# Kernel tuning notes

Measured on AMD Instinct MI355X. Metric: run time of the kernel, lower is better.

The kernel has to match this reference:

```python
import jax, jax.numpy as jnp
from jax import lax
import numpy as np

P = 2          # cost exponent: C(x,y) = |x-y|^p / p
BLUR = 0.05    # final epsilon = BLUR**P
SCALING = 0.5  # geomloss epsilon-scaling factor


def _cost(x, y):
    # squared Euclidean distance / 2  (geomloss p=2 cost), shape [N, M]
    sq = jnp.sum(x * x, axis=1)[:, None] + jnp.sum(y * y, axis=1)[None, :] - 2.0 * (x @ y.T)
    return jnp.maximum(sq, 0.0) * 0.5


def _softmin(eps, C, h):
    # h: log-weights (+ potential/eps) over columns of C; returns [rows]
    return -eps * jax.nn.logsumexp(h[None, :] - C / eps, axis=1)


def setup_inputs() -> dict:
    key = jax.random.key(0)
    k1, k2 = jax.random.split(key)
    N, M, D = 8192, 8192, 64
    g = jax.random.normal(k1, (N, D), jnp.float32)
    Y = jax.random.normal(k2, (M, D), jnp.float32) + 1.0  # shifted target measure
    # geomloss epsilon_schedule: diameter**p annealed by SCALING**p down to BLUR**p
    xy = np.concatenate([np.asarray(g), np.asarray(Y)], axis=0)
    diameter = float(np.linalg.norm(xy.max(0) - xy.min(0)))
    eps_list = ([diameter ** P]
                + [float(np.exp(e)) for e in np.arange(P * np.log(diameter), P * np.log(BLUR), P * np.log(SCALING))]
                + [BLUR ** P])
    return {"g": g, "Y": Y, "eps_list": jnp.asarray(eps_list, jnp.float32)}


def reference(g, Y, eps_list):
    x, y = g, Y
    N, M = x.shape[0], y.shape[0]
    a_log = jnp.full((N,), -jnp.log(jnp.float32(N)), x.dtype)  # uniform log-weights
    b_log = jnp.full((M,), -jnp.log(jnp.float32(M)), y.dtype)

    C_xy, C_yx = _cost(x, y), _cost(y, x)
    C_xx, C_yy = _cost(x, x), _cost(y, y)
    # Sinkhorn loop runs on detached costs (geomloss runs it under no_grad)
    sg = lax.stop_gradient
    Cxy_s, Cyx_s, Cxx_s, Cyy_s = sg(C_xy), sg(C_yx), sg(C_xx), sg(C_yy)

    eps0 = eps_list[0]
    f_aa = _softmin(eps0, Cxx_s, a_log)
    g_bb = _softmin(eps0, Cyy_s, b_log)
    g_ab = _softmin(eps0, Cyx_s, a_log)
    f_ba = _softmin(eps0, Cxy_s, b_log)

    def step(carry, eps):
        f_aa, g_bb, g_ab, f_ba = carry
        ft = _softmin(eps, Cxy_s, b_log + g_ab / eps)
        gt = _softmin(eps, Cyx_s, a_log + f_ba / eps)
        ftaa = _softmin(eps, Cxx_s, a_log + f_aa / eps)
        gtbb = _softmin(eps, Cyy_s, b_log + g_bb / eps)
        # symmetrized (averaged) dual updates, as in geomloss
        return (0.5 * (f_aa + ftaa), 0.5 * (g_bb + gtbb),
                0.5 * (g_ab + gt), 0.5 * (f_ba + ft)), None

    (f_aa, g_bb, g_ab, f_ba), _ = lax.scan(step, (f_aa, g_bb, g_ab, f_ba), eps_list)

    # last extrapolation at eps = blur**p: differentiable costs, detached potentials
    eps = eps_list[-1]
    f_ba_f = _softmin(eps, C_xy, sg(b_log + g_ab / eps))
    g_ab_f = _softmin(eps, C_yx, sg(a_log + f_ba / eps))
    f_aa_f = _softmin(eps, C_xx, sg(a_log + f_aa / eps))
    g_bb_f = _softmin(eps, C_yy, sg(b_log + g_bb / eps))

    # S_eps(alpha, beta) = <alpha, f_ba - f_aa> + <beta, g_ab - g_bb> (uniform weights)
    return jnp.mean(f_ba_f - f_aa_f) + jnp.mean(g_ab_f - g_bb_f)
```

## Files before the change

### kernel.cpp

```cpp
#include <hip/hip_runtime.h>
#include <math.h>

#define D 64
#define BR 128
#define NCHUNK 16
#define YLD 72
#define LOG2E 1.4426950408889634f
#define LN2   0.6931471805599453f

typedef __attribute__((ext_vector_type(8))) __bf16 bf16x8;
typedef __attribute__((ext_vector_type(4))) float  floatx4;
typedef __attribute__((ext_vector_type(2))) float  floatx2;

static __device__ __forceinline__ float exp2fast(float x) {
#if __has_builtin(__builtin_amdgcn_exp2f)
    return __builtin_amdgcn_exp2f(x);
#else
    return exp2f(x);
#endif
}
static __device__ __forceinline__ float log2fast(float x) {
#if __has_builtin(__builtin_amdgcn_logf)
    return __builtin_amdgcn_logf(x);
#else
    return log2f(x);
#endif
}
static __device__ __forceinline__ float max3f(float a, float b, float c) {
    return fmaxf(fmaxf(a, b), c);
}

static __device__ __forceinline__ unsigned short f2bf_rne(float f) {
    unsigned u = __float_as_uint(f);
    return (unsigned short)((u + 0x7fffu + ((u >> 16) & 1u)) >> 16);
}

struct OpDesc {
    const unsigned short* xh;
    const unsigned short* yh;
    const float* cc;
    const float* sqn_col;
    float* pm; float* ps;
    int n_rows, n_cols, symmetric, pad;
};
struct P4 { OpDesc op[4]; };

struct MDesc {
    const float* pm; const float* ps;
    const float* sqn_row;
    const float* oldpot;
    float* newpot;
    float* ccout;
    float wlog_c;
    int n_rows, mix, pad;
};
struct M4 { MDesc op[4]; };

__global__ void cvt_kernel(const float* __restrict__ x,
                           unsigned short* __restrict__ xh, int n_elem8)
{
    int i = blockIdx.x * blockDim.x + threadIdx.x;
    if (i >= n_elem8) return;
    const float4* xp = (const float4*)x;
    float4 v0 = xp[i * 2], v1 = xp[i * 2 + 1];
    float v[8] = {v0.x, v0.y, v0.z, v0.w, v1.x, v1.y, v1.z, v1.w};
    unsigned h[8];
#pragma unroll
    for (int k = 0; k < 8; ++k) h[k] = f2bf_rne(v[k]);
    uint4 ph;
    ph.x = h[0] | (h[1] << 16); ph.y = h[2] | (h[3] << 16);
    ph.z = h[4] | (h[5] << 16); ph.w = h[6] | (h[7] << 16);
    ((uint4*)xh)[i] = ph;
}

__global__ void sqnorm_kernel(const float* __restrict__ x, float* __restrict__ sqn, int n)
{
    int i = blockIdx.x * blockDim.x + threadIdx.x;
    if (i >= n) return;
    const float4* xp = (const float4*)(x + (size_t)i * D);
    float sum = 0.0f;
#pragma unroll
    for (int k = 0; k < D / 4; ++k) {
        float4 v = xp[k];
        sum += v.x * v.x + v.y * v.y + v.z * v.z + v.w * v.w;
    }
    sqn[i] = 0.5f * sum;
}

__global__ void init_cc_kernel(const float* __restrict__ sqn_x, const float* __restrict__ sqn_y,
                               float* cc0, float* cc1, float* cc2, float* cc3,
                               const float* __restrict__ eps_list,
                               float a_log, float b_log, int N, int M)
{
    int i = blockIdx.x * blockDim.x + threadIdx.x;
    float inv_e0 = 1.0f / eps_list[0];
    if (i < M) { float v = (b_log - sqn_y[i] * inv_e0) * LOG2E; cc0[i] = v; cc3[i] = v; }
    if (i < N) { float v = (a_log - sqn_x[i] * inv_e0) * LOG2E; cc1[i] = v; cc2[i] = v; }
}

__global__ __launch_bounds__(256)
void softmin_mfma4(P4 p4, const float* __restrict__ eps_list, int eps_idx)
{
    __shared__ __bf16 yth[128 * YLD];

    const OpDesc o = p4.op[blockIdx.z];
    const int t    = threadIdx.x;
    const int lane = t & 63;
    const int w    = t >> 6;
    const int lx   = lane & 15;
    const int q    = lane >> 4;
    const int row0 = blockIdx.x * BR;
    const int chunk = blockIdx.y;
    const int cols_per_chunk = o.n_cols / NCHUNK;
    const int nsub = cols_per_chunk / 128;

    const float eps     = eps_list[eps_idx];
    const float inv_eps = 1.0f / eps;
    const float scale2  = inv_eps * LOG2E;
    const floatx2 s2v   = (floatx2){scale2, scale2};
    const floatx4 Z4    = (floatx4){0.f, 0.f, 0.f, 0.f};

    bf16x8 ah[2][2];
    {
        const int r0 = row0 + w * 32;
#pragma unroll
        for (int rt = 0; rt < 2; ++rt)
#pragma unroll
            for (int ks = 0; ks < 2; ++ks)
                ah[rt][ks] = *(const bf16x8*)(o.xh + (size_t)(r0 + rt * 16 + lx) * D + ks * 32 + q * 8);
    }

    const int diag_blk = o.symmetric && ((row0 / cols_per_chunk) == chunk);
    float sqr[8];
    if (diag_blk) {
#pragma unroll
        for (int idx = 0; idx < 8; ++idx) {
            int row = row0 + w * 32 + (idx >> 2) * 16 + q * 4 + (idx & 3);
            sqr[idx] = o.sqn_col[row];
        }
    }

    float m[8], s[8];
#pragma unroll
    for (int i = 0; i < 8; ++i) { m[i] = -__builtin_inff(); s[i] = 0.0f; }

    for (int sub = 0; sub < nsub; ++sub) {
        const int col0 = chunk * cols_per_chunk + sub * 128;

        __syncthreads();
        {
            const uint4* gh = (const uint4*)(o.yh + (size_t)col0 * D);
#pragma unroll
            for (int i = 0; i < 4; ++i) {
                int c = t + i * 256;
                int row = c >> 3, part = c & 7;
                uint4 vh = gh[c];
                *(uint4*)(&yth[row * YLD + part * 8]) = vh;
            }
        }
        __syncthreads();

        float cc[8];
#pragma unroll
        for (int ct = 0; ct < 8; ++ct) cc[ct] = o.cc[col0 + ct * 16 + lx];

        floatx4 acc[8][2];
#pragma unroll
        for (int ct = 0; ct < 8; ++ct) {
            const int cl = ct * 16 + lx;
            bf16x8 bh0 = *(const bf16x8*)&yth[cl * YLD + q * 8];
            bf16x8 bh1 = *(const bf16x8*)&yth[cl * YLD + 32 + q * 8];
#pragma unroll
            for (int rt = 0; rt < 2; ++rt) {
                floatx4 a = __builtin_amdgcn_mfma_f32_16x16x32_bf16(ah[rt][0], bh0, Z4, 0, 0, 0);
                acc[ct][rt] = __builtin_amdgcn_mfma_f32_16x16x32_bf16(ah[rt][1], bh1, a, 0, 0, 0);
            }
        }

        if (diag_blk && col0 == row0) {
#pragma unroll
            for (int rt = 0; rt < 2; ++rt)
#pragma unroll
                for (int r = 0; r < 4; ++r) {
                    if (lx == q * 4 + r) {
                        const float v = 2.0f * sqr[rt * 4 + r];
#pragma unroll
                        for (int ct = 0; ct < 8; ++ct)
                            if (ct == w * 2 + rt) acc[ct][rt][r] = v;
                    }
                }
        }

        floatx2 ccv[4];
#pragma unroll
        for (int cp = 0; cp < 4; ++cp)
            ccv[cp] = (floatx2){cc[cp * 2], cc[cp * 2 + 1]};

#pragma unroll
        for (int rt = 0; rt < 2; ++rt)
#pragma unroll
            for (int r = 0; r < 4; ++r) {
                const int idx = rt * 4 + r;
                floatx2 zv[4];
#pragma unroll
                for (int cp = 0; cp < 4; ++cp) {
                    floatx2 av = (floatx2){acc[cp * 2][rt][r], acc[cp * 2 + 1][rt][r]};
                    zv[cp] = __builtin_elementwise_fma(av, s2v, ccv[cp]);
                }
                float M = max3f(zv[0].x, zv[0].y, zv[1].x);
                M = max3f(M, zv[1].y, zv[2].x);
                M = max3f(M, zv[2].y, zv[3].x);
                M = max3f(M, zv[3].y, m[idx]);
                const floatx2 Mv = (floatx2){M, M};
                floatx2 sv = (floatx2){0.f, 0.f};
#pragma unroll
                for (int cp = 0; cp < 4; ++cp) {
                    floatx2 d = zv[cp] - Mv;
                    sv += (floatx2){exp2fast(d.x), exp2fast(d.y)};
                }
                s[idx] = fmaf(s[idx], exp2fast(m[idx] - M), sv.x + sv.y);
                m[idx] = M;
            }
    }

#pragma unroll
    for (int idx = 0; idx < 8; ++idx) {
        float mm = m[idx], ss = s[idx];
#pragma unroll
        for (int d = 1; d < 16; d <<= 1) {
            float mo = __shfl_xor(mm, d, 64);
            float so = __shfl_xor(ss, d, 64);
            float M = fmaxf(mm, mo);
            ss = ss * exp2fast(mm - M) + so * exp2fast(mo - M);
            mm = M;
        }
        m[idx] = mm; s[idx] = ss;
    }
    if (lx == 0) {
#pragma unroll
        for (int idx = 0; idx < 8; ++idx) {
            const int rt = idx >> 2, r = idx & 3;
            const int row = row0 + w * 32 + rt * 16 + q * 4 + r;
            o.pm[chunk * o.n_rows + row] = m[idx];
            o.ps[chunk * o.n_rows + row] = s[idx];
        }
    }
}

__global__ void softmin_merge4(M4 m4, const float* __restrict__ eps_list,
                               int eps_idx, int eps_idx_next)
{
    const MDesc o = m4.op[blockIdx.y];
    int i = blockIdx.x * blockDim.x + threadIdx.x;
    if (i >= o.n_rows) return;
    const float eps = eps_list[eps_idx];
    float M = -__builtin_inff();
    for (int c = 0; c < NCHUNK; ++c) M = fmaxf(M, o.pm[c * o.n_rows + i]);
    float S = 0.0f;
    for (int c = 0; c < NCHUNK; ++c) S += o.ps[c * o.n_rows + i] * exp2fast(o.pm[c * o.n_rows + i] - M);
    const float sq = o.sqn_row[i];
    float val = sq - eps * LN2 * (M + log2fast(S));
    float nv = o.mix ? 0.5f * (o.oldpot[i] + val) : val;
    o.newpot[i] = nv;
    if (o.ccout) {
        float inv_en = 1.0f / eps_list[eps_idx_next];
        o.ccout[i] = (o.wlog_c + (nv - sq) * inv_en) * LOG2E;
    }
}

__global__ void final_reduce(const float* __restrict__ f_ba_f, const float* __restrict__ f_aa_f,
                             const float* __restrict__ g_ab_f, const float* __restrict__ g_bb_f,
                             int n, int mcount, float* __restrict__ out)
{
    __shared__ float red[256];
    float s1 = 0.0f, s2 = 0.0f;
    for (int i = threadIdx.x; i < n; i += 256)      s1 += (f_ba_f[i] - f_aa_f[i]);
    for (int i = threadIdx.x; i < mcount; i += 256) s2 += (g_ab_f[i] - g_bb_f[i]);
    red[threadIdx.x] = s1 / (float)n + s2 / (float)mcount;
    __syncthreads();
    for (int off = 128; off > 0; off >>= 1) {
        if (threadIdx.x < off) red[threadIdx.x] += red[threadIdx.x + off];
        __syncthreads();
    }
    if (threadIdx.x == 0) out[0] = red[0];
}

extern "C" void kernel_launch(void* const* d_in, const int* in_sizes, int n_in,
                              void* d_out, int out_size, void* d_ws, size_t ws_size,
                              hipStream_t stream)
{
    const float* g        = (const float*)d_in[0];
    const float* Y        = (const float*)d_in[1];
    const float* eps_list = (const float*)d_in[2];
    const int N = in_sizes[0] / D;
    const int M = in_sizes[1] / D;
    const int L = in_sizes[2];
    const float a_log = -logf((float)N);
    const float b_log = -logf((float)M);
    const int NM = (N > M) ? N : M;
    const size_t PMS = (size_t)NCHUNK * NM;

    unsigned short* us = (unsigned short*)d_ws;
    unsigned short* gxh = us; us += (size_t)N * D;
    unsigned short* gyh = us; us += (size_t)M * D;

    float* ws = (float*)us;
    float* sqn_x = ws; ws += N;
    float* sqn_y = ws; ws += M;
    float* fba[2]; fba[0] = ws; ws += N; fba[1] = ws; ws += N;
    float* gab[2]; gab[0] = ws; ws += M; gab[1] = ws; ws += M;
    float* fa[2];  fa[0]  = ws; ws += N; fa[1]  = ws; ws += N;
    float* gb[2];  gb[0]  = ws; ws += M; gb[1]  = ws; ws += M;
    float* f_ba_f = ws; ws += N;
    float* g_ab_f = ws; ws += M;
    float* f_aa_f = ws; ws += N;
    float* g_bb_f = ws; ws += M;
    float* cc[2][4];
    for (int pbuf = 0; pbuf < 2; ++pbuf)
        for (int i = 0; i < 4; ++i) { cc[pbuf][i] = ws; ws += NM; }
    float* pm = ws; ws += 4 * PMS;
    float* psb = ws; ws += 4 * PMS;

    sqnorm_kernel<<<(N + 255) / 256, 256, 0, stream>>>(g, sqn_x, N);
    sqnorm_kernel<<<(M + 255) / 256, 256, 0, stream>>>(Y, sqn_y, M);
    cvt_kernel<<<(N * D / 8 + 255) / 256, 256, 0, stream>>>(g, gxh, N * D / 8);
    cvt_kernel<<<(M * D / 8 + 255) / 256, 256, 0, stream>>>(Y, gyh, M * D / 8);
    init_cc_kernel<<<(NM + 255) / 256, 256, 0, stream>>>(sqn_x, sqn_y,
        cc[0][0], cc[0][1], cc[0][2], cc[0][3], eps_list, a_log, b_log, N, M);

    auto phase = [&](int eidx, int eidx_next, int mix, int cur, int ccp, int writecc,
                     float* out0, float* out1, float* out2, float* out3) {
        P4 p;
        p.op[0] = { gxh, gyh, cc[ccp][0], sqn_y, pm + 0 * PMS, psb + 0 * PMS, N, M, 0, 0 };
        p.op[1] = { gyh, gxh, cc[ccp][1], sqn_x, pm + 1 * PMS, psb + 1 * PMS, M, N, 0, 0 };
        p.op[2] = { gxh, gxh, cc[ccp][2], sqn_x, pm + 2 * PMS, psb + 2 * PMS, N, N, 1, 0 };
        p.op[3] = { gyh, gyh, cc[ccp][3], sqn_y, pm + 3 * PMS, psb + 3 * PMS, M, M, 1, 0 };
        softmin_mfma4<<<dim3(NM / BR, NCHUNK, 4), 256, 0, stream>>>(p, eps_list, eidx);

        M4 mm;
        mm.op[0] = { pm + 0 * PMS, psb + 0 * PMS, sqn_x, fba[cur], out0,
                     writecc ? cc[ccp ^ 1][1] : nullptr, a_log, N, mix, 0 };
        mm.op[1] = { pm + 1 * PMS, psb + 1 * PMS, sqn_y, gab[cur], out1,
                     writecc ? cc[ccp ^ 1][0] : nullptr, b_log, M, mix, 0 };
        mm.op[2] = { pm + 2 * PMS, psb + 2 * PMS, sqn_x, fa[cur], out2,
                     writecc ? cc[ccp ^ 1][2] : nullptr, a_log, N, mix, 0 };
        mm.op[3] = { pm + 3 * PMS, psb + 3 * PMS, sqn_y, gb[cur], out3,
                     writecc ? cc[ccp ^ 1][3] : nullptr, b_log, M, mix, 0 };
        softmin_merge4<<<dim3((NM + 255) / 256, 4), 256, 0, stream>>>(mm, eps_list, eidx, eidx_next);
    };

    phase(0, 0, 0, 0, 0, 1, fba[0], gab[0], fa[0], gb[0]);
    int cur = 0, ccp = 1;

    for (int k = 0; k < L; ++k) {
        int en = (k + 1 < L) ? (k + 1) : (L - 1);
        phase(k, en, 1, cur, ccp, 1, fba[cur ^ 1], gab[cur ^ 1], fa[cur ^ 1], gb[cur ^ 1]);
        cur ^= 1; ccp ^= 1;
    }

    phase(L - 1, L - 1, 0, cur, ccp, 0, f_ba_f, g_ab_f, f_aa_f, g_bb_f);

    final_reduce<<<1, 256, 0, stream>>>(f_ba_f, f_aa_f, g_ab_f, g_bb_f, N, M, (float*)d_out);
}
```

Before: 1.290 ms.

## Skip negligible softmin chunks using bounds from previous iteration's potentials

```diff
diff --git a/kernel.cpp b/kernel.cpp
--- a/kernel.cpp
+++ b/kernel.cpp
@@ -7,6 +7,7 @@
 #define YLD 72
 #define LOG2E 1.4426950408889634f
 #define LN2   0.6931471805599453f
+#define SAFE_MARGIN 200.0f
 
 typedef __attribute__((ext_vector_type(8))) __bf16 bf16x8;
 typedef __attribute__((ext_vector_type(4))) float  floatx4;
@@ -41,6 +42,8 @@
     const float* cc;
     const float* sqn_col;
     float* pm; float* ps;
+    const int* keep;
+    float wlog_col;
     int n_rows, n_cols, symmetric, pad;
 };
 struct P4 { OpDesc op[4]; };
@@ -51,6 +54,7 @@
     const float* oldpot;
     float* newpot;
     float* ccout;
+    float* dpout;
     float wlog_c;
     int n_rows, mix, pad;
 };
@@ -98,19 +102,86 @@
     if (i < N) { float v = (a_log - sqn_x[i] * inv_e0) * LOG2E; cc1[i] = v; cc2[i] = v; }
 }
 
+__global__ void plan_chunk(const float* __restrict__ dp0, const float* __restrict__ dp1,
+                           const float* __restrict__ dp2, const float* __restrict__ dp3,
+                           float* __restrict__ dmax, float* __restrict__ dmin,
+                           int c0, int c1, int c2, int c3)
+{
+    __shared__ float smx[256], smn[256];
+    const int op = blockIdx.y, c = blockIdx.x, t = threadIdx.x;
+    const float* dp = (op == 0) ? dp0 : (op == 1) ? dp1 : (op == 2) ? dp2 : dp3;
+    const int nc = (op == 0) ? c0 : (op == 1) ? c1 : (op == 2) ? c2 : c3;
+    const int cpc = nc / NCHUNK;
+    float mx = -__builtin_inff(), mn = __builtin_inff();
+    for (int i = t; i < cpc; i += 256) {
+        float v = dp[c * cpc + i];
+        mx = fmaxf(mx, v); mn = fminf(mn, v);
+    }
+    smx[t] = mx; smn[t] = mn;
+    __syncthreads();
+    for (int off = 128; off > 0; off >>= 1) {
+        if (t < off) { smx[t] = fmaxf(smx[t], smx[t + off]); smn[t] = fminf(smn[t], smn[t + off]); }
+        __syncthreads();
+    }
+    if (t == 0) { dmax[op * NCHUNK + c] = smx[0]; dmin[op * NCHUNK + c] = smn[0]; }
+}
+
+__global__ void plan_keep(P4 p4, const float* __restrict__ eps_list, int eps_prev, int eps_cur,
+                          const float* __restrict__ dmax, const float* __restrict__ dmin,
+                          int* __restrict__ keepbuf, int rbmax, int trust_all)
+{
+    __shared__ int flags[NCHUNK];
+    const int op = blockIdx.y, rb = blockIdx.x, t = threadIdx.x;
+    const OpDesc o = p4.op[op];
+    if (rb >= o.n_rows / BR) return;
+    const int row = rb * BR + t;
+    int* kb = keepbuf + ((size_t)op * rbmax + rb) * NCHUNK;
+
+    const float ep = eps_list[eps_prev], ec = eps_list[eps_cur];
+    const float r = ep / ec;
+    const float base = LOG2E * (1.0f - r) * o.wlog_col;
+    const float sc = LOG2E / ec;
+
+    float up[NCHUNK];
+    float glb = -__builtin_inff();
+#pragma unroll
+    for (int c = 0; c < NCHUNK; ++c) {
+        const int oldk = trust_all ? 1 : kb[c];
+        const float pmv = o.pm[c * o.n_rows + row];
+        up[c] = r * pmv + base + dmax[op * NCHUNK + c] * sc;
+        if (oldk) {
+            float lo = r * pmv + base + dmin[op * NCHUNK + c] * sc;
+            glb = fmaxf(glb, lo);
+        }
+    }
+    if (t < NCHUNK) flags[t] = 0;
+    __syncthreads();
+    const float thr = glb - SAFE_MARGIN;
+#pragma unroll
+    for (int c = 0; c < NCHUNK; ++c)
+        if (up[c] >= thr) flags[c] = 1;
+    __syncthreads();
+#pragma unroll
+    for (int c = 0; c < NCHUNK; ++c)
+        if (!flags[c]) { o.pm[c * o.n_rows + row] = up[c]; o.ps[c * o.n_rows + row] = 0.0f; }
+    if (t < NCHUNK) kb[t] = flags[t];
+}
+
 __global__ __launch_bounds__(256)
 void softmin_mfma4(P4 p4, const float* __restrict__ eps_list, int eps_idx)
 {
     __shared__ __bf16 yth[128 * YLD];
 
     const OpDesc o = p4.op[blockIdx.z];
+    const int chunk = blockIdx.y;
+    if (o.keep && o.keep[blockIdx.x * NCHUNK + chunk] == 0) return;
+
     const int t    = threadIdx.x;
     const int lane = t & 63;
     const int w    = t >> 6;
     const int lx   = lane & 15;
     const int q    = lane >> 4;
     const int row0 = blockIdx.x * BR;
-    const int chunk = blockIdx.y;
     const int cols_per_chunk = o.n_cols / NCHUNK;
     const int nsub = cols_per_chunk / 128;
 
@@ -215,8 +286,8 @@
                 floatx2 sv = (floatx2){0.f, 0.f};
 #pragma unroll
                 for (int cp = 0; cp < 4; ++cp) {
-                    floatx2 d = zv[cp] - Mv;
-                    sv += (floatx2){exp2fast(d.x), exp2fast(d.y)};
+                    floatx2 dd = zv[cp] - Mv;
+                    sv += (floatx2){exp2fast(dd.x), exp2fast(dd.y)};
                 }
                 s[idx] = fmaf(s[idx], exp2fast(m[idx] - M), sv.x + sv.y);
                 m[idx] = M;
@@ -234,15 +305,11 @@
             ss = ss * exp2fast(mm - M) + so * exp2fast(mo - M);
             mm = M;
         }
-        m[idx] = mm; s[idx] = ss;
-    }
-    if (lx == 0) {
-#pragma unroll
-        for (int idx = 0; idx < 8; ++idx) {
+        if (lx == 0) {
             const int rt = idx >> 2, r = idx & 3;
             const int row = row0 + w * 32 + rt * 16 + q * 4 + r;
-            o.pm[chunk * o.n_rows + row] = m[idx];
-            o.ps[chunk * o.n_rows + row] = s[idx];
+            o.pm[chunk * o.n_rows + row] = mm;
+            o.ps[chunk * o.n_rows + row] = ss;
         }
     }
 }
@@ -260,12 +327,14 @@
     for (int c = 0; c < NCHUNK; ++c) S += o.ps[c * o.n_rows + i] * exp2fast(o.pm[c * o.n_rows + i] - M);
     const float sq = o.sqn_row[i];
     float val = sq - eps * LN2 * (M + log2fast(S));
-    float nv = o.mix ? 0.5f * (o.oldpot[i] + val) : val;
+    float pold = o.mix ? o.oldpot[i] : 0.0f;
+    float nv = o.mix ? 0.5f * (pold + val) : val;
     o.newpot[i] = nv;
     if (o.ccout) {
         float inv_en = 1.0f / eps_list[eps_idx_next];
         o.ccout[i] = (o.wlog_c + (nv - sq) * inv_en) * LOG2E;
     }
+    if (o.dpout) o.dpout[i] = nv - pold;
 }
 
 __global__ void final_reduce(const float* __restrict__ f_ba_f, const float* __restrict__ f_aa_f,
@@ -298,6 +367,7 @@
     const float a_log = -logf((float)N);
     const float b_log = -logf((float)M);
     const int NM = (N > M) ? N : M;
+    const int rbmax = NM / BR;
     const size_t PMS = (size_t)NCHUNK * NM;
 
     unsigned short* us = (unsigned short*)d_ws;
@@ -318,8 +388,13 @@
     float* cc[2][4];
     for (int pbuf = 0; pbuf < 2; ++pbuf)
         for (int i = 0; i < 4; ++i) { cc[pbuf][i] = ws; ws += NM; }
+    float* dpc[4];
+    for (int i = 0; i < 4; ++i) { dpc[i] = ws; ws += NM; }
+    float* dmax = ws; ws += 4 * NCHUNK;
+    float* dmin = ws; ws += 4 * NCHUNK;
     float* pm = ws; ws += 4 * PMS;
     float* psb = ws; ws += 4 * PMS;
+    int* keepbuf = (int*)ws;
 
     sqnorm_kernel<<<(N + 255) / 256, 256, 0, stream>>>(g, sqn_x, N);
     sqnorm_kernel<<<(M + 255) / 256, 256, 0, stream>>>(Y, sqn_y, M);
@@ -329,36 +404,50 @@
         cc[0][0], cc[0][1], cc[0][2], cc[0][3], eps_list, a_log, b_log, N, M);
 
     auto phase = [&](int eidx, int eidx_next, int mix, int cur, int ccp, int writecc,
-                     float* out0, float* out1, float* out2, float* out3) {
+                     float* out0, float* out1, float* out2, float* out3,
+                     int use_plan, int eps_prev, int trust_all) {
         P4 p;
-        p.op[0] = { gxh, gyh, cc[ccp][0], sqn_y, pm + 0 * PMS, psb + 0 * PMS, N, M, 0, 0 };
-        p.op[1] = { gyh, gxh, cc[ccp][1], sqn_x, pm + 1 * PMS, psb + 1 * PMS, M, N, 0, 0 };
-        p.op[2] = { gxh, gxh, cc[ccp][2], sqn_x, pm + 2 * PMS, psb + 2 * PMS, N, N, 1, 0 };
-        p.op[3] = { gyh, gyh, cc[ccp][3], sqn_y, pm + 3 * PMS, psb + 3 * PMS, M, M, 1, 0 };
+        const int* k0 = use_plan ? keepbuf + 0 * (size_t)rbmax * NCHUNK : nullptr;
+        const int* k1 = use_plan ? keepbuf + 1 * (size_t)rbmax * NCHUNK : nullptr;
+        const int* k2 = use_plan ? keepbuf + 2 * (size_t)rbmax * NCHUNK : nullptr;
+        const int* k3 = use_plan ? keepbuf + 3 * (size_t)rbmax * NCHUNK : nullptr;
+        p.op[0] = { gxh, gyh, cc[ccp][0], sqn_y, pm + 0 * PMS, psb + 0 * PMS, k0, b_log, N, M, 0, 0 };
+        p.op[1] = { gyh, gxh, cc[ccp][1], sqn_x, pm + 1 * PMS, psb + 1 * PMS, k1, a_log, M, N, 0, 0 };
+        p.op[2] = { gxh, gxh, cc[ccp][2], sqn_x, pm + 2 * PMS, psb + 2 * PMS, k2, a_log, N, N, 1, 0 };
+        p.op[3] = { gyh, gyh, cc[ccp][3], sqn_y, pm + 3 * PMS, psb + 3 * PMS, k3, b_log, M, M, 1, 0 };
+
+        if (use_plan) {
+            plan_chunk<<<dim3(NCHUNK, 4), 256, 0, stream>>>(dpc[0], dpc[1], dpc[2], dpc[3],
+                                                            dmax, dmin, M, N, N, M);
+            plan_keep<<<dim3(rbmax, 4), 128, 0, stream>>>(p, eps_list, eps_prev, eidx,
+                                                          dmax, dmin, keepbuf, rbmax, trust_all);
+        }
         softmin_mfma4<<<dim3(NM / BR, NCHUNK, 4), 256, 0, stream>>>(p, eps_list, eidx);
 
         M4 mm;
         mm.op[0] = { pm + 0 * PMS, psb + 0 * PMS, sqn_x, fba[cur], out0,
-                     writecc ? cc[ccp ^ 1][1] : nullptr, a_log, N, mix, 0 };
+                     writecc ? cc[ccp ^ 1][1] : nullptr, writecc ? dpc[1] : nullptr, a_log, N, mix, 0 };
         mm.op[1] = { pm + 1 * PMS, psb + 1 * PMS, sqn_y, gab[cur], out1,
-                     writecc ? cc[ccp ^ 1][0] : nullptr, b_log, M, mix, 0 };
+                     writecc ? cc[ccp ^ 1][0] : nullptr, writecc ? dpc[0] : nullptr, b_log, M, mix, 0 };
         mm.op[2] = { pm + 2 * PMS, psb + 2 * PMS, sqn_x, fa[cur], out2,
-                     writecc ? cc[ccp ^ 1][2] : nullptr, a_log, N, mix, 0 };
+                     writecc ? cc[ccp ^ 1][2] : nullptr, writecc ? dpc[2] : nullptr, a_log, N, mix, 0 };
         mm.op[3] = { pm + 3 * PMS, psb + 3 * PMS, sqn_y, gb[cur], out3,
-                     writecc ? cc[ccp ^ 1][3] : nullptr, b_log, M, mix, 0 };
+                     writecc ? cc[ccp ^ 1][3] : nullptr, writecc ? dpc[3] : nullptr, b_log, M, mix, 0 };
         softmin_merge4<<<dim3((NM + 255) / 256, 4), 256, 0, stream>>>(mm, eps_list, eidx, eidx_next);
     };
 
-    phase(0, 0, 0, 0, 0, 1, fba[0], gab[0], fa[0], gb[0]);
+    phase(0, 0, 0, 0, 0, 1, fba[0], gab[0], fa[0], gb[0], 0, 0, 0);
     int cur = 0, ccp = 1;
 
     for (int k = 0; k < L; ++k) {
         int en = (k + 1 < L) ? (k + 1) : (L - 1);
-        phase(k, en, 1, cur, ccp, 1, fba[cur ^ 1], gab[cur ^ 1], fa[cur ^ 1], gb[cur ^ 1]);
+        int eprev = (k == 0) ? 0 : (k - 1);
+        phase(k, en, 1, cur, ccp, 1, fba[cur ^ 1], gab[cur ^ 1], fa[cur ^ 1], gb[cur ^ 1],
+              1, eprev, (k == 0) ? 1 : 0);
         cur ^= 1; ccp ^= 1;
     }
 
-    phase(L - 1, L - 1, 0, cur, ccp, 0, f_ba_f, g_ab_f, f_aa_f, g_bb_f);
+    phase(L - 1, L - 1, 0, cur, ccp, 0, f_ba_f, g_ab_f, f_aa_f, g_bb_f, 1, L - 1, 0);
 
     final_reduce<<<1, 256, 0, stream>>>(f_ba_f, f_aa_f, g_ab_f, g_bb_f, N, M, (float*)d_out);
 }
```

Result: no change. 1.286 ms (-0.3%).
